# Performance work log

Hardware: AMD Instinct MI355X
Metric: run time of the kernel (lower is better)

Reference implementation:

```python
import jax, jax.numpy as jnp
import numpy as np

N = 20000        # nodes
E = 320000       # directed edges (before self-loops)
HEADS = 4
IN_DIM = 256
HID = [256, 128]
ZD = [128, 64]
S = 10           # num_samples in reparameterize
REAL_MIN = 2.2e-10
THETA_MAX = 1000.0
KMIN, KMAX = 0.1, 1000.0
SLOPE = 0.2      # GATConv leaky_relu negative_slope


def setup_inputs() -> dict:
    key = jax.random.key(0)
    ks = jax.random.split(key, 24)
    f32 = jnp.float32
    def p(k, shape, scale):
        return jax.random.normal(k, shape, dtype=f32) * scale
    inp = {}
    inp["x"] = jax.random.normal(ks[0], (N, IN_DIM), dtype=f32)
    inp["edge_index"] = jax.random.randint(ks[1], (2, E), 0, N)
    # layer 0: GAT 256 -> 4 heads x 64 (concat = 256)
    inp["gatW0"] = p(ks[2], (HID[0], IN_DIM), 0.06)
    inp["asrc0"] = p(ks[3], (HEADS, HID[0] // HEADS), 0.1)
    inp["adst0"] = p(ks[4], (HEADS, HID[0] // HEADS), 0.1)
    inp["gatb0"] = p(ks[5], (HID[0],), 0.02)
    inp["fcW0"] = p(ks[6], (ZD[0], HID[0]), 0.06)
    inp["fcb0"] = p(ks[7], (ZD[0],), 0.02)
    inp["shW0"] = p(ks[8], (ZD[0], ZD[0]), 0.08)
    inp["shb0"] = p(ks[9], (ZD[0],), 0.02)
    inp["scW0"] = p(ks[10], (ZD[0], ZD[0]), 0.08)
    inp["scb0"] = p(ks[11], (ZD[0],), 0.02)
    # layer 1: GAT 256 -> 4 heads x 32 (concat = 128)
    inp["gatW1"] = p(ks[12], (HID[1], HID[0]), 0.06)
    inp["asrc1"] = p(ks[13], (HEADS, HID[1] // HEADS), 0.1)
    inp["adst1"] = p(ks[14], (HEADS, HID[1] // HEADS), 0.1)
    inp["gatb1"] = p(ks[15], (HID[1],), 0.02)
    inp["fcW1"] = p(ks[16], (ZD[1], HID[1]), 0.06)
    inp["fcb1"] = p(ks[17], (ZD[1],), 0.02)
    inp["shW1"] = p(ks[18], (ZD[1], ZD[1]), 0.08)
    inp["shb1"] = p(ks[19], (ZD[1],), 0.02)
    inp["scW1"] = p(ks[20], (ZD[1], ZD[1]), 0.08)
    inp["scb1"] = p(ks[21], (ZD[1],), 0.02)
    # Weibull reparameterization noise eps ~ U(0,1), shape (S, z_dim, N)
    inp["eps0"] = jax.random.uniform(ks[22], (S, ZD[0], N), dtype=f32)
    inp["eps1"] = jax.random.uniform(ks[23], (S, ZD[1], N), dtype=f32)
    return inp


def _gat(x, src, dst, W, a_src, a_dst, b):
    """PyG GATConv (shared lin, concat heads, add_self_loops done by caller)."""
    n = x.shape[0]
    xw = (x @ W.T).reshape(n, HEADS, -1)            # [N, H, C]
    s = (xw * a_src[None]).sum(-1)                  # [N, H] alpha_src
    d = (xw * a_dst[None]).sum(-1)                  # [N, H] alpha_dst
    e = s[src] + d[dst]                             # [E, H]
    e = jnp.where(e > 0, e, SLOPE * e)              # leaky_relu
    m = jax.lax.stop_gradient(jax.ops.segment_max(e, dst, num_segments=n))
    ex = jnp.exp(e - m[dst])
    den = jax.ops.segment_sum(ex, dst, num_segments=n)
    alpha = ex / (den[dst] + 1e-16)                 # segment softmax over in-edges
    out = jax.ops.segment_sum(alpha[:, :, None] * xw[src], dst, num_segments=n)
    return out.reshape(n, -1) + b                   # [N, H*C]


def _reparam(k, l, eps):
    # theta = l * (-log(max(1-eps, real_min)))^(1/k), mean over samples, clamp
    lm = jnp.log(jnp.maximum(1.0 - eps, REAL_MIN))  # [S, z, N]
    theta = l[None] * jnp.power(-lm, 1.0 / k[None])
    return jnp.clip(theta.mean(0), REAL_MIN, THETA_MAX)


def _right(h, Wk, bk, Wl, bl, eps):
    k = jnp.clip(jax.nn.softplus(h @ Wk.T + bk).T, KMIN, KMAX)      # [z, N]
    l = jnp.maximum(jax.nn.softplus(h @ Wl.T + bl).T, REAL_MIN)     # [z, N]
    l = l / jnp.exp(jax.lax.lgamma(1.0 + 1.0 / k))
    return _reparam(k, l, eps), k, l


def reference(x, edge_index, gatW0, asrc0, adst0, gatb0, fcW0, fcb0, shW0, shb0,
              scW0, scb0, gatW1, asrc1, adst1, gatb1, fcW1, fcb1, shW1, shb1,
              scW1, scb1, eps0, eps1):
    n = x.shape[0]
    loops = jnp.arange(n)
    src = jnp.concatenate([edge_index[0], loops])   # GATConv add_self_loops
    dst = jnp.concatenate([edge_index[1], loops])
    h0 = _gat(x, src, dst, gatW0, asrc0, adst0, gatb0)
    z0 = jax.nn.softplus(h0 @ fcW0.T + fcb0)
    h1 = _gat(h0, src, dst, gatW1, asrc1, adst1, gatb1)
    z1 = jax.nn.softplus(h1 @ fcW1.T + fcb1)
    theta1, k1, l1 = _right(z1, shW1, shb1, scW1, scb1, eps1)
    theta0, k0, l0 = _right(z0, shW0, shb0, scW0, scb0, eps0)
    return (theta0, theta1, k0, k1, l0, l1)
```

## Files before the change

### kernel.cpp

```cpp
#include <hip/hip_runtime.h>
#include <math.h>

#define N_NODES 20000
#define E_EDGES 320000
#define NHEADS 4
#define RMIN 2.2e-10f
#define THETA_MAX 1000.0f
#define SLOPE 0.2f

__device__ __forceinline__ float softplus_f(float x) {
    return fmaxf(x, 0.0f) + log1pf(expf(-fabsf(x)));
}

__global__ __launch_bounds__(256) void count_kernel(const int* __restrict__ dst,
                                                    int* __restrict__ deg) {
    int e = blockIdx.x * 256 + threadIdx.x;
    if (e < E_EDGES) atomicAdd(&deg[dst[e]], 1);
}

__global__ __launch_bounds__(256) void scan_kernel(const int* __restrict__ deg,
                                                   int* __restrict__ rowptr,
                                                   int* __restrict__ cursor) {
    __shared__ int part[256];
    int t = threadIdx.x;
    const int CH = (N_NODES + 255) / 256;
    int base = t * CH;
    int sum = 0;
    for (int i = 0; i < CH; ++i) {
        int idx = base + i;
        if (idx < N_NODES) sum += deg[idx];
    }
    part[t] = sum;
    __syncthreads();
    for (int off = 1; off < 256; off <<= 1) {
        int v = (t >= off) ? part[t - off] : 0;
        __syncthreads();
        part[t] += v;
        __syncthreads();
    }
    int run = (t == 0) ? 0 : part[t - 1];
    for (int i = 0; i < CH; ++i) {
        int idx = base + i;
        if (idx < N_NODES) {
            rowptr[idx] = run;
            cursor[idx] = run;
            run += deg[idx];
        }
    }
    if (t == 255) rowptr[N_NODES] = run;
}

__global__ __launch_bounds__(256) void scatter_kernel(const int* __restrict__ src,
                                                      const int* __restrict__ dst,
                                                      int* __restrict__ cursor,
                                                      int* __restrict__ csr) {
    int e = blockIdx.x * 256 + threadIdx.x;
    if (e < E_EDGES) {
        int p = atomicAdd(&cursor[dst[e]], 1);
        csr[p] = src[e];
    }
}

template <int MODE, bool TRANS>
__global__ __launch_bounds__(256) void gemm_kernel(const float* __restrict__ A,
                                                   const float* __restrict__ W,
                                                   const float* __restrict__ bias,
                                                   float* __restrict__ out,
                                                   int M, int K, int NO) {
    __shared__ float As[16][68];
    __shared__ float Bs[16][68];
    int tid = threadIdx.x;
    int tx = tid & 15, ty = tid >> 4;
    int bm = blockIdx.x * 64;
    int bn = blockIdx.y * 64;
    float acc[4][4] = {};
    for (int k0 = 0; k0 < K; k0 += 16) {
        {
            int m = tid >> 2;
            int kk0 = (tid & 3) * 4;
            int row = bm + m;
            float4 v = make_float4(0.f, 0.f, 0.f, 0.f);
            if (row < M) v = *(const float4*)(A + (size_t)row * K + k0 + kk0);
            As[kk0 + 0][m] = v.x; As[kk0 + 1][m] = v.y;
            As[kk0 + 2][m] = v.z; As[kk0 + 3][m] = v.w;
        }
        {
            int o = tid >> 2;
            int kk0 = (tid & 3) * 4;
            float4 v = *(const float4*)(W + (size_t)(bn + o) * K + k0 + kk0);
            Bs[kk0 + 0][o] = v.x; Bs[kk0 + 1][o] = v.y;
            Bs[kk0 + 2][o] = v.z; Bs[kk0 + 3][o] = v.w;
        }
        __syncthreads();
#pragma unroll
        for (int kk = 0; kk < 16; ++kk) {
            float a[4], b[4];
            *(float4*)a = *(const float4*)(&As[kk][ty * 4]);
            *(float4*)b = *(const float4*)(&Bs[kk][tx * 4]);
#pragma unroll
            for (int i = 0; i < 4; ++i)
#pragma unroll
                for (int j = 0; j < 4; ++j) acc[i][j] += a[i] * b[j];
        }
        __syncthreads();
    }
    int r0 = bm + ty * 4;
    int c0 = bn + tx * 4;
    float bv[4] = {0.f, 0.f, 0.f, 0.f};
    if (MODE != 0) *(float4*)bv = *(const float4*)(bias + c0);
    float vals[4][4];
#pragma unroll
    for (int i = 0; i < 4; ++i)
#pragma unroll
        for (int j = 0; j < 4; ++j) {
            float v = acc[i][j];
            if (MODE == 1) v = softplus_f(v + bv[j]);
            else if (MODE == 2) { v = softplus_f(v + bv[j]); v = fminf(fmaxf(v, 0.1f), 1000.0f); }
            else if (MODE == 3) { v = fmaxf(softplus_f(v + bv[j]), RMIN); }
            vals[i][j] = v;
        }
    if (!TRANS) {
#pragma unroll
        for (int i = 0; i < 4; ++i) {
            int row = r0 + i;
            if (row < M) *(float4*)(out + (size_t)row * NO + c0) = *(float4*)vals[i];
        }
    } else {
        if (r0 + 3 < M) {
#pragma unroll
            for (int j = 0; j < 4; ++j) {
                float col[4] = {vals[0][j], vals[1][j], vals[2][j], vals[3][j]};
                *(float4*)(out + (size_t)(c0 + j) * M + r0) = *(float4*)col;
            }
        } else {
#pragma unroll
            for (int i = 0; i < 4; ++i) {
                int row = r0 + i;
                if (row < M)
#pragma unroll
                    for (int j = 0; j < 4; ++j) out[(size_t)(c0 + j) * M + row] = vals[i][j];
            }
        }
    }
}

template <int F, int CPER>
__global__ __launch_bounds__(256) void sd_kernel(const float* __restrict__ xw,
                                                 const float* __restrict__ asrc,
                                                 const float* __restrict__ adst,
                                                 float* __restrict__ s,
                                                 float* __restrict__ d) {
    int wave = threadIdx.x >> 6;
    int lane = threadIdx.x & 63;
    int n = blockIdx.x * 4 + wave;
    if (n >= N_NODES) return;
    float ss[NHEADS] = {0, 0, 0, 0}, dd[NHEADS] = {0, 0, 0, 0};
#pragma unroll
    for (int j = 0; j < F / 64; ++j) {
        int c = j * 64 + lane;
        int h = c / CPER;
        int cc = c % CPER;
        float v = xw[(size_t)n * F + c];
        ss[h] += v * asrc[h * CPER + cc];
        dd[h] += v * adst[h * CPER + cc];
    }
#pragma unroll
    for (int off = 32; off > 0; off >>= 1) {
#pragma unroll
        for (int h = 0; h < NHEADS; ++h) {
            ss[h] += __shfl_xor(ss[h], off, 64);
            dd[h] += __shfl_xor(dd[h], off, 64);
        }
    }
    if (lane == 0) {
#pragma unroll
        for (int h = 0; h < NHEADS; ++h) {
            s[n * NHEADS + h] = ss[h];
            d[n * NHEADS + h] = dd[h];
        }
    }
}

template <int F, int CPER>
__global__ __launch_bounds__(256) void agg_kernel(const float* __restrict__ xw,
                                                  const float* __restrict__ s,
                                                  const float* __restrict__ d,
                                                  const int* __restrict__ rowptr,
                                                  const int* __restrict__ csr,
                                                  const float* __restrict__ bias,
                                                  float* __restrict__ out) {
    int wave = threadIdx.x >> 6;
    int lane = threadIdx.x & 63;
    int n = blockIdx.x * 4 + wave;
    if (n >= N_NODES) return;
    constexpr int J = F / 64;
    float dh[NHEADS], shh[NHEADS];
#pragma unroll
    for (int h = 0; h < NHEADS; ++h) {
        dh[h] = d[n * NHEADS + h];
        shh[h] = s[n * NHEADS + h];
    }
    float den[NHEADS], w[NHEADS], acc[J];
#pragma unroll
    for (int h = 0; h < NHEADS; ++h) {
        float e = shh[h] + dh[h];
        e = e > 0.f ? e : SLOPE * e;
        w[h] = expf(e);
        den[h] = w[h];
    }
#pragma unroll
    for (int j = 0; j < J; ++j) {
        int c = j * 64 + lane;
        acc[j] = w[c / CPER] * xw[(size_t)n * F + c];
    }
    int beg = rowptr[n], end = rowptr[n + 1];
    for (int idx = beg; idx < end; ++idx) {
        int srcn = csr[idx];
#pragma unroll
        for (int h = 0; h < NHEADS; ++h) {
            float e = s[srcn * NHEADS + h] + dh[h];
            e = e > 0.f ? e : SLOPE * e;
            w[h] = expf(e);
            den[h] += w[h];
        }
#pragma unroll
        for (int j = 0; j < J; ++j) {
            int c = j * 64 + lane;
            acc[j] += w[c / CPER] * xw[(size_t)srcn * F + c];
        }
    }
#pragma unroll
    for (int j = 0; j < J; ++j) {
        int c = j * 64 + lane;
        out[(size_t)n * F + c] = acc[j] / (den[c / CPER] + 1e-16f) + bias[c];
    }
}

__global__ __launch_bounds__(256) void theta_kernel(const float* __restrict__ eps,
                                                    const float* __restrict__ kptr,
                                                    float* __restrict__ lptr,
                                                    float* __restrict__ theta, int ZN) {
    int i = blockIdx.x * 256 + threadIdx.x;
    if (i >= ZN) return;
    float k = kptr[i];
    float invk = 1.0f / k;
    float lg = expf(lgammaf(1.0f + invk));
    float l = lptr[i] / lg;
    lptr[i] = l;
    float acc = 0.0f;
#pragma unroll
    for (int ss = 0; ss < 10; ++ss) {
        float u = eps[(size_t)ss * ZN + i];
        float v = -logf(fmaxf(1.0f - u, RMIN));
        acc += exp2f(log2f(v) * invk);
    }
    float th = l * acc * 0.1f;
    th = fminf(fmaxf(th, RMIN), THETA_MAX);
    theta[i] = th;
}

extern "C" void kernel_launch(void* const* d_in, const int* in_sizes, int n_in,
                              void* d_out, int out_size, void* d_ws, size_t ws_size,
                              hipStream_t stream) {
    const float* x     = (const float*)d_in[0];
    const int*   eidx  = (const int*)d_in[1];
    const float* gatW0 = (const float*)d_in[2];
    const float* asrc0 = (const float*)d_in[3];
    const float* adst0 = (const float*)d_in[4];
    const float* gatb0 = (const float*)d_in[5];
    const float* fcW0  = (const float*)d_in[6];
    const float* fcb0  = (const float*)d_in[7];
    const float* shW0  = (const float*)d_in[8];
    const float* shb0  = (const float*)d_in[9];
    const float* scW0  = (const float*)d_in[10];
    const float* scb0  = (const float*)d_in[11];
    const float* gatW1 = (const float*)d_in[12];
    const float* asrc1 = (const float*)d_in[13];
    const float* adst1 = (const float*)d_in[14];
    const float* gatb1 = (const float*)d_in[15];
    const float* fcW1  = (const float*)d_in[16];
    const float* fcb1  = (const float*)d_in[17];
    const float* shW1  = (const float*)d_in[18];
    const float* shb1  = (const float*)d_in[19];
    const float* scW1  = (const float*)d_in[20];
    const float* scb1  = (const float*)d_in[21];
    const float* eps0  = (const float*)d_in[22];
    const float* eps1  = (const float*)d_in[23];

    const int* e_src = eidx;
    const int* e_dst = eidx + E_EDGES;

    size_t off = 0;
    auto carve = [&](size_t elems) {
        void* p = (char*)d_ws + off;
        off += ((elems * 4 + 255) / 256) * 256;
        return p;
    };
    float* xw0 = (float*)carve(20000u * 256);
    float* h0  = (float*)carve(20000u * 256);
    float* z0  = (float*)carve(20000u * 128);
    float* xw1 = (float*)carve(20000u * 128);
    float* h1  = (float*)carve(20000u * 128);
    float* z1  = (float*)carve(20000u * 64);
    float* s0  = (float*)carve(20000u * 4);
    float* d0  = (float*)carve(20000u * 4);
    float* s1  = (float*)carve(20000u * 4);
    float* d1  = (float*)carve(20000u * 4);
    int* deg    = (int*)carve(20000);
    int* rowptr = (int*)carve(20001);
    int* cursor = (int*)carve(20000);
    int* csr    = (int*)carve(E_EDGES);

    float* out    = (float*)d_out;
    float* theta0 = out;
    float* theta1 = out + 2560000;
    float* k0     = out + 3840000;
    float* k1     = out + 6400000;
    float* l0     = out + 7680000;
    float* l1     = out + 10240000;

    const int M = N_NODES;
    dim3 blk(256);

    (void)hipMemsetAsync(deg, 0, N_NODES * sizeof(int), stream);
    count_kernel<<<(E_EDGES + 255) / 256, blk, 0, stream>>>(e_dst, deg);
    scan_kernel<<<1, blk, 0, stream>>>(deg, rowptr, cursor);
    scatter_kernel<<<(E_EDGES + 255) / 256, blk, 0, stream>>>(e_src, e_dst, cursor, csr);

    gemm_kernel<0, false><<<dim3(313, 4), blk, 0, stream>>>(x, gatW0, nullptr, xw0, M, 256, 256);
    sd_kernel<256, 64><<<5000, blk, 0, stream>>>(xw0, asrc0, adst0, s0, d0);
    agg_kernel<256, 64><<<5000, blk, 0, stream>>>(xw0, s0, d0, rowptr, csr, gatb0, h0);
    gemm_kernel<1, false><<<dim3(313, 2), blk, 0, stream>>>(h0, fcW0, fcb0, z0, M, 256, 128);

    gemm_kernel<0, false><<<dim3(313, 2), blk, 0, stream>>>(h0, gatW1, nullptr, xw1, M, 256, 128);
    sd_kernel<128, 32><<<5000, blk, 0, stream>>>(xw1, asrc1, adst1, s1, d1);
    agg_kernel<128, 32><<<5000, blk, 0, stream>>>(xw1, s1, d1, rowptr, csr, gatb1, h1);
    gemm_kernel<1, false><<<dim3(313, 1), blk, 0, stream>>>(h1, fcW1, fcb1, z1, M, 128, 64);

    gemm_kernel<2, true><<<dim3(313, 2), blk, 0, stream>>>(z0, shW0, shb0, k0, M, 128, 128);
    gemm_kernel<3, true><<<dim3(313, 2), blk, 0, stream>>>(z0, scW0, scb0, l0, M, 128, 128);
    gemm_kernel<2, true><<<dim3(313, 1), blk, 0, stream>>>(z1, shW1, shb1, k1, M, 64, 64);
    gemm_kernel<3, true><<<dim3(313, 1), blk, 0, stream>>>(z1, scW1, scb1, l1, M, 64, 64);

    theta_kernel<<<(2560000 + 255) / 256, blk, 0, stream>>>(eps0, k0, l0, theta0, 2560000);
    theta_kernel<<<(1280000 + 255) / 256, blk, 0, stream>>>(eps1, k1, l1, theta1, 1280000);
}
```

Baseline: 693.0 us.

## Enlarge GEMM tiles, vectorize GAT score/aggregation and theta kernels with fast math

The GEMM kernel moves to 128-row tiles with 8xTN register blocking, so each thread does more FMAs per shared-memory load and fewer blocks are launched. The attention score kernel now has each lane load a float4 or float2 and reduce within 16-lane head groups. The aggregation kernel gives each lane one head and a vector of features, and unrolls two edges per iteration to put more gathers in flight. The theta kernel handles four elements per thread with vector loads and uses __expf/__logf intrinsics, trading some accuracy for cheaper transcendentals.

Measured after the change: 729.9 us. 1.05x slower.

```diff
diff --git a/kernel.cpp b/kernel.cpp
--- a/kernel.cpp
+++ b/kernel.cpp
@@ -61,58 +61,84 @@
     }
 }
 
-template <int MODE, bool TRANS>
-__global__ __launch_bounds__(256) void gemm_kernel(const float* __restrict__ A,
-                                                   const float* __restrict__ W,
-                                                   const float* __restrict__ bias,
-                                                   float* __restrict__ out,
-                                                   int M, int K, int NO) {
-    __shared__ float As[16][68];
-    __shared__ float Bs[16][68];
+template <int MODE, bool TRANS, int BN>
+__global__ __launch_bounds__(256) void gemm_big(const float* __restrict__ A,
+                                                const float* __restrict__ W,
+                                                const float* __restrict__ bias,
+                                                float* __restrict__ out,
+                                                int M, int K, int NO) {
+    constexpr int TN = BN / 16;
+    __shared__ float As[16][132];
+    __shared__ float Bs[16][BN + 4];
     int tid = threadIdx.x;
     int tx = tid & 15, ty = tid >> 4;
-    int bm = blockIdx.x * 64;
-    int bn = blockIdx.y * 64;
-    float acc[4][4] = {};
+    int bm = blockIdx.x * 128;
+    int bn = blockIdx.y * BN;
+    float acc[8][TN] = {};
+
+    int am = tid >> 1;
+    int ak = (tid & 1) * 8;
+    int arow = bm + am;
+    bool aval = arow < M;
+    const float* Arow = A + (size_t)arow * K + ak;
+
+    int bo, bk;
+    if (BN == 128) { bo = tid >> 1; bk = (tid & 1) * 8; }
+    else           { bo = tid >> 2; bk = (tid & 3) * 4; }
+    const float* Wrow = W + (size_t)(bn + bo) * K + bk;
+
     for (int k0 = 0; k0 < K; k0 += 16) {
-        {
-            int m = tid >> 2;
-            int kk0 = (tid & 3) * 4;
-            int row = bm + m;
-            float4 v = make_float4(0.f, 0.f, 0.f, 0.f);
-            if (row < M) v = *(const float4*)(A + (size_t)row * K + k0 + kk0);
-            As[kk0 + 0][m] = v.x; As[kk0 + 1][m] = v.y;
-            As[kk0 + 2][m] = v.z; As[kk0 + 3][m] = v.w;
-        }
-        {
-            int o = tid >> 2;
-            int kk0 = (tid & 3) * 4;
-            float4 v = *(const float4*)(W + (size_t)(bn + o) * K + k0 + kk0);
-            Bs[kk0 + 0][o] = v.x; Bs[kk0 + 1][o] = v.y;
-            Bs[kk0 + 2][o] = v.z; Bs[kk0 + 3][o] = v.w;
+        float4 a0 = make_float4(0.f, 0.f, 0.f, 0.f), a1 = a0;
+        if (aval) {
+            a0 = *(const float4*)(Arow + k0);
+            a1 = *(const float4*)(Arow + k0 + 4);
+        }
+        As[ak + 0][am] = a0.x; As[ak + 1][am] = a0.y;
+        As[ak + 2][am] = a0.z; As[ak + 3][am] = a0.w;
+        As[ak + 4][am] = a1.x; As[ak + 5][am] = a1.y;
+        As[ak + 6][am] = a1.z; As[ak + 7][am] = a1.w;
+        if (BN == 128) {
+            float4 b0 = *(const float4*)(Wrow + k0);
+            float4 b1 = *(const float4*)(Wrow + k0 + 4);
+            Bs[bk + 0][bo] = b0.x; Bs[bk + 1][bo] = b0.y;
+            Bs[bk + 2][bo] = b0.z; Bs[bk + 3][bo] = b0.w;
+            Bs[bk + 4][bo] = b1.x; Bs[bk + 5][bo] = b1.y;
+            Bs[bk + 6][bo] = b1.z; Bs[bk + 7][bo] = b1.w;
+        } else {
+            float4 b0 = *(const float4*)(Wrow + k0);
+            Bs[bk + 0][bo] = b0.x; Bs[bk + 1][bo] = b0.y;
+            Bs[bk + 2][bo] = b0.z; Bs[bk + 3][bo] = b0.w;
         }
         __syncthreads();
 #pragma unroll
         for (int kk = 0; kk < 16; ++kk) {
-            float a[4], b[4];
-            *(float4*)a = *(const float4*)(&As[kk][ty * 4]);
-            *(float4*)b = *(const float4*)(&Bs[kk][tx * 4]);
-#pragma unroll
-            for (int i = 0; i < 4; ++i)
-#pragma unroll
-                for (int j = 0; j < 4; ++j) acc[i][j] += a[i] * b[j];
+            float a[8], b[TN];
+            *(float4*)(a) = *(const float4*)(&As[kk][ty * 8]);
+            *(float4*)(a + 4) = *(const float4*)(&As[kk][ty * 8 + 4]);
+            *(float4*)(b) = *(const float4*)(&Bs[kk][tx * TN]);
+            if (TN == 8) *(float4*)(b + 4) = *(const float4*)(&Bs[kk][tx * TN + 4]);
+#pragma unroll
+            for (int i = 0; i < 8; ++i)
+#pragma unroll
+                for (int j = 0; j < TN; ++j) acc[i][j] += a[i] * b[j];
         }
         __syncthreads();
     }
-    int r0 = bm + ty * 4;
-    int c0 = bn + tx * 4;
-    float bv[4] = {0.f, 0.f, 0.f, 0.f};
-    if (MODE != 0) *(float4*)bv = *(const float4*)(bias + c0);
-    float vals[4][4];
-#pragma unroll
-    for (int i = 0; i < 4; ++i)
-#pragma unroll
-        for (int j = 0; j < 4; ++j) {
+
+    int r0 = bm + ty * 8;
+    int c0 = bn + tx * TN;
+    float bv[TN];
+#pragma unroll
+    for (int j = 0; j < TN; ++j) bv[j] = 0.f;
+    if (MODE != 0) {
+        *(float4*)(bv) = *(const float4*)(bias + c0);
+        if (TN == 8) *(float4*)(bv + 4) = *(const float4*)(bias + c0 + 4);
+    }
+    float vals[8][TN];
+#pragma unroll
+    for (int i = 0; i < 8; ++i)
+#pragma unroll
+        for (int j = 0; j < TN; ++j) {
             float v = acc[i][j];
             if (MODE == 1) v = softplus_f(v + bv[j]);
             else if (MODE == 2) { v = softplus_f(v + bv[j]); v = fminf(fmaxf(v, 0.1f), 1000.0f); }
@@ -121,30 +147,35 @@
         }
     if (!TRANS) {
 #pragma unroll
-        for (int i = 0; i < 4; ++i) {
+        for (int i = 0; i < 8; ++i) {
             int row = r0 + i;
-            if (row < M) *(float4*)(out + (size_t)row * NO + c0) = *(float4*)vals[i];
+            if (row < M) {
+                *(float4*)(out + (size_t)row * NO + c0) = *(float4*)(vals[i]);
+                if (TN == 8) *(float4*)(out + (size_t)row * NO + c0 + 4) = *(float4*)(vals[i] + 4);
+            }
         }
     } else {
-        if (r0 + 3 < M) {
-#pragma unroll
-            for (int j = 0; j < 4; ++j) {
-                float col[4] = {vals[0][j], vals[1][j], vals[2][j], vals[3][j]};
-                *(float4*)(out + (size_t)(c0 + j) * M + r0) = *(float4*)col;
+        if (r0 + 7 < M) {
+#pragma unroll
+            for (int j = 0; j < TN; ++j) {
+                float c0v[4] = {vals[0][j], vals[1][j], vals[2][j], vals[3][j]};
+                float c1v[4] = {vals[4][j], vals[5][j], vals[6][j], vals[7][j]};
+                *(float4*)(out + (size_t)(c0 + j) * M + r0) = *(float4*)c0v;
+                *(float4*)(out + (size_t)(c0 + j) * M + r0 + 4) = *(float4*)c1v;
             }
         } else {
 #pragma unroll
-            for (int i = 0; i < 4; ++i) {
+            for (int i = 0; i < 8; ++i) {
                 int row = r0 + i;
                 if (row < M)
 #pragma unroll
-                    for (int j = 0; j < 4; ++j) out[(size_t)(c0 + j) * M + row] = vals[i][j];
+                    for (int j = 0; j < TN; ++j) out[(size_t)(c0 + j) * M + row] = vals[i][j];
             }
         }
     }
 }
 
-template <int F, int CPER>
+template <int F>
 __global__ __launch_bounds__(256) void sd_kernel(const float* __restrict__ xw,
                                                  const float* __restrict__ asrc,
                                                  const float* __restrict__ adst,
@@ -154,34 +185,33 @@
     int lane = threadIdx.x & 63;
     int n = blockIdx.x * 4 + wave;
     if (n >= N_NODES) return;
-    float ss[NHEADS] = {0, 0, 0, 0}, dd[NHEADS] = {0, 0, 0, 0};
-#pragma unroll
-    for (int j = 0; j < F / 64; ++j) {
-        int c = j * 64 + lane;
-        int h = c / CPER;
-        int cc = c % CPER;
-        float v = xw[(size_t)n * F + c];
-        ss[h] += v * asrc[h * CPER + cc];
-        dd[h] += v * adst[h * CPER + cc];
-    }
-#pragma unroll
-    for (int off = 32; off > 0; off >>= 1) {
-#pragma unroll
-        for (int h = 0; h < NHEADS; ++h) {
-            ss[h] += __shfl_xor(ss[h], off, 64);
-            dd[h] += __shfl_xor(dd[h], off, 64);
-        }
-    }
-    if (lane == 0) {
-#pragma unroll
-        for (int h = 0; h < NHEADS; ++h) {
-            s[n * NHEADS + h] = ss[h];
-            d[n * NHEADS + h] = dd[h];
-        }
-    }
-}
-
-template <int F, int CPER>
+    float ss, dd;
+    if (F == 256) {
+        float4 v = *(const float4*)(xw + (size_t)n * 256 + lane * 4);
+        float4 as = *(const float4*)(asrc + lane * 4);
+        float4 ad = *(const float4*)(adst + lane * 4);
+        ss = v.x * as.x + v.y * as.y + v.z * as.z + v.w * as.w;
+        dd = v.x * ad.x + v.y * ad.y + v.z * ad.z + v.w * ad.w;
+    } else {
+        float2 v = *(const float2*)(xw + (size_t)n * 128 + lane * 2);
+        float2 as = *(const float2*)(asrc + lane * 2);
+        float2 ad = *(const float2*)(adst + lane * 2);
+        ss = v.x * as.x + v.y * as.y;
+        dd = v.x * ad.x + v.y * ad.y;
+    }
+#pragma unroll
+    for (int off = 8; off > 0; off >>= 1) {
+        ss += __shfl_xor(ss, off, 64);
+        dd += __shfl_xor(dd, off, 64);
+    }
+    if ((lane & 15) == 0) {
+        int h = lane >> 4;
+        s[n * NHEADS + h] = ss;
+        d[n * NHEADS + h] = dd;
+    }
+}
+
+template <int F>
 __global__ __launch_bounds__(256) void agg_kernel(const float* __restrict__ xw,
                                                   const float* __restrict__ s,
                                                   const float* __restrict__ d,
@@ -193,46 +223,79 @@
     int lane = threadIdx.x & 63;
     int n = blockIdx.x * 4 + wave;
     if (n >= N_NODES) return;
-    constexpr int J = F / 64;
-    float dh[NHEADS], shh[NHEADS];
-#pragma unroll
-    for (int h = 0; h < NHEADS; ++h) {
-        dh[h] = d[n * NHEADS + h];
-        shh[h] = s[n * NHEADS + h];
-    }
-    float den[NHEADS], w[NHEADS], acc[J];
-#pragma unroll
-    for (int h = 0; h < NHEADS; ++h) {
-        float e = shh[h] + dh[h];
-        e = e > 0.f ? e : SLOPE * e;
-        w[h] = expf(e);
-        den[h] = w[h];
-    }
-#pragma unroll
-    for (int j = 0; j < J; ++j) {
-        int c = j * 64 + lane;
-        acc[j] = w[c / CPER] * xw[(size_t)n * F + c];
-    }
+    int h = lane >> 4;
+    float dh = d[n * 4 + h];
+    float eself = s[n * 4 + h] + dh;
+    eself = eself > 0.f ? eself : SLOPE * eself;
+    float wself = __expf(eself);
+    float den = wself;
+
     int beg = rowptr[n], end = rowptr[n + 1];
-    for (int idx = beg; idx < end; ++idx) {
-        int srcn = csr[idx];
-#pragma unroll
-        for (int h = 0; h < NHEADS; ++h) {
-            float e = s[srcn * NHEADS + h] + dh[h];
-            e = e > 0.f ? e : SLOPE * e;
-            w[h] = expf(e);
-            den[h] += w[h];
-        }
-#pragma unroll
-        for (int j = 0; j < J; ++j) {
-            int c = j * 64 + lane;
-            acc[j] += w[c / CPER] * xw[(size_t)srcn * F + c];
-        }
-    }
-#pragma unroll
-    for (int j = 0; j < J; ++j) {
-        int c = j * 64 + lane;
-        out[(size_t)n * F + c] = acc[j] / (den[c / CPER] + 1e-16f) + bias[c];
+    if (F == 256) {
+        const float4* xw4 = (const float4*)xw;
+        float4 v = xw4[(size_t)n * 64 + lane];
+        float4 acc = make_float4(wself * v.x, wself * v.y, wself * v.z, wself * v.w);
+        int idx = beg;
+        for (; idx + 1 < end; idx += 2) {
+            int s0 = csr[idx], s1 = csr[idx + 1];
+            float e0 = s[s0 * 4 + h] + dh;
+            float e1 = s[s1 * 4 + h] + dh;
+            e0 = e0 > 0.f ? e0 : SLOPE * e0;
+            e1 = e1 > 0.f ? e1 : SLOPE * e1;
+            float w0 = __expf(e0);
+            float w1 = __expf(e1);
+            float4 v0 = xw4[(size_t)s0 * 64 + lane];
+            float4 v1 = xw4[(size_t)s1 * 64 + lane];
+            den += w0 + w1;
+            acc.x += w0 * v0.x; acc.y += w0 * v0.y; acc.z += w0 * v0.z; acc.w += w0 * v0.w;
+            acc.x += w1 * v1.x; acc.y += w1 * v1.y; acc.z += w1 * v1.z; acc.w += w1 * v1.w;
+        }
+        if (idx < end) {
+            int s0 = csr[idx];
+            float e0 = s[s0 * 4 + h] + dh;
+            e0 = e0 > 0.f ? e0 : SLOPE * e0;
+            float w0 = __expf(e0);
+            float4 v0 = xw4[(size_t)s0 * 64 + lane];
+            den += w0;
+            acc.x += w0 * v0.x; acc.y += w0 * v0.y; acc.z += w0 * v0.z; acc.w += w0 * v0.w;
+        }
+        float inv = 1.0f / (den + 1e-16f);
+        float4 bv = *(const float4*)(bias + lane * 4);
+        float4 o = make_float4(acc.x * inv + bv.x, acc.y * inv + bv.y,
+                               acc.z * inv + bv.z, acc.w * inv + bv.w);
+        *(float4*)(out + (size_t)n * 256 + lane * 4) = o;
+    } else {
+        const float2* xw2 = (const float2*)xw;
+        float2 v = xw2[(size_t)n * 64 + lane];
+        float2 acc = make_float2(wself * v.x, wself * v.y);
+        int idx = beg;
+        for (; idx + 1 < end; idx += 2) {
+            int s0 = csr[idx], s1 = csr[idx + 1];
+            float e0 = s[s0 * 4 + h] + dh;
+            float e1 = s[s1 * 4 + h] + dh;
+            e0 = e0 > 0.f ? e0 : SLOPE * e0;
+            e1 = e1 > 0.f ? e1 : SLOPE * e1;
+            float w0 = __expf(e0);
+            float w1 = __expf(e1);
+            float2 v0 = xw2[(size_t)s0 * 64 + lane];
+            float2 v1 = xw2[(size_t)s1 * 64 + lane];
+            den += w0 + w1;
+            acc.x += w0 * v0.x; acc.y += w0 * v0.y;
+            acc.x += w1 * v1.x; acc.y += w1 * v1.y;
+        }
+        if (idx < end) {
+            int s0 = csr[idx];
+            float e0 = s[s0 * 4 + h] + dh;
+            e0 = e0 > 0.f ? e0 : SLOPE * e0;
+            float w0 = __expf(e0);
+            float2 v0 = xw2[(size_t)s0 * 64 + lane];
+            den += w0;
+            acc.x += w0 * v0.x; acc.y += w0 * v0.y;
+        }
+        float inv = 1.0f / (den + 1e-16f);
+        float2 bv = *(const float2*)(bias + lane * 2);
+        float2 o = make_float2(acc.x * inv + bv.x, acc.y * inv + bv.y);
+        *(float2*)(out + (size_t)n * 128 + lane * 2) = o;
     }
 }
 
@@ -240,23 +303,39 @@
                                                     const float* __restrict__ kptr,
                                                     float* __restrict__ lptr,
                                                     float* __restrict__ theta, int ZN) {
-    int i = blockIdx.x * 256 + threadIdx.x;
-    if (i >= ZN) return;
-    float k = kptr[i];
-    float invk = 1.0f / k;
-    float lg = expf(lgammaf(1.0f + invk));
-    float l = lptr[i] / lg;
-    lptr[i] = l;
-    float acc = 0.0f;
+    int idx = blockIdx.x * 256 + threadIdx.x;
+    int base = idx * 4;
+    if (base >= ZN) return;
+    float4 k4 = *(const float4*)(kptr + base);
+    float4 l4 = *(const float4*)(lptr + base);
+    float kk[4] = {k4.x, k4.y, k4.z, k4.w};
+    float ll[4] = {l4.x, l4.y, l4.z, l4.w};
+    float invk[4], acc[4];
+#pragma unroll
+    for (int c = 0; c < 4; ++c) {
+        invk[c] = 1.0f / kk[c];
+        ll[c] = ll[c] / __expf(lgammaf(1.0f + invk[c]));
+        acc[c] = 0.0f;
+    }
 #pragma unroll
     for (int ss = 0; ss < 10; ++ss) {
-        float u = eps[(size_t)ss * ZN + i];
-        float v = -logf(fmaxf(1.0f - u, RMIN));
-        acc += exp2f(log2f(v) * invk);
-    }
-    float th = l * acc * 0.1f;
-    th = fminf(fmaxf(th, RMIN), THETA_MAX);
-    theta[i] = th;
+        float4 u4 = *(const float4*)(eps + (size_t)ss * ZN + base);
+        float uu[4] = {u4.x, u4.y, u4.z, u4.w};
+#pragma unroll
+        for (int c = 0; c < 4; ++c) {
+            float w = fmaxf(1.0f - uu[c], RMIN);
+            float v = -__logf(w);
+            acc[c] += __expf(invk[c] * __logf(v));
+        }
+    }
+    float th[4];
+#pragma unroll
+    for (int c = 0; c < 4; ++c) {
+        float t = ll[c] * acc[c] * 0.1f;
+        th[c] = fminf(fmaxf(t, RMIN), THETA_MAX);
+    }
+    *(float4*)(theta + base) = make_float4(th[0], th[1], th[2], th[3]);
+    *(float4*)(lptr + base) = make_float4(ll[0], ll[1], ll[2], ll[3]);
 }
 
 extern "C" void kernel_launch(void* const* d_in, const int* in_sizes, int n_in,
@@ -327,21 +406,21 @@
     scan_kernel<<<1, blk, 0, stream>>>(deg, rowptr, cursor);
     scatter_kernel<<<(E_EDGES + 255) / 256, blk, 0, stream>>>(e_src, e_dst, cursor, csr);
 
-    gemm_kernel<0, false><<<dim3(313, 4), blk, 0, stream>>>(x, gatW0, nullptr, xw0, M, 256, 256);
-    sd_kernel<256, 64><<<5000, blk, 0, stream>>>(xw0, asrc0, adst0, s0, d0);
-    agg_kernel<256, 64><<<5000, blk, 0, stream>>>(xw0, s0, d0, rowptr, csr, gatb0, h0);
-    gemm_kernel<1, false><<<dim3(313, 2), blk, 0, stream>>>(h0, fcW0, fcb0, z0, M, 256, 128);
-
-    gemm_kernel<0, false><<<dim3(313, 2), blk, 0, stream>>>(h0, gatW1, nullptr, xw1, M, 256, 128);
-    sd_kernel<128, 32><<<5000, blk, 0, stream>>>(xw1, asrc1, adst1, s1, d1);
-    agg_kernel<128, 32><<<5000, blk, 0, stream>>>(xw1, s1, d1, rowptr, csr, gatb1, h1);
-    gemm_kernel<1, false><<<dim3(313, 1), blk, 0, stream>>>(h1, fcW1, fcb1, z1, M, 128, 64);
-
-    gemm_kernel<2, true><<<dim3(313, 2), blk, 0, stream>>>(z0, shW0, shb0, k0, M, 128, 128);
-    gemm_kernel<3, true><<<dim3(313, 2), blk, 0, stream>>>(z0, scW0, scb0, l0, M, 128, 128);
-    gemm_kernel<2, true><<<dim3(313, 1), blk, 0, stream>>>(z1, shW1, shb1, k1, M, 64, 64);
-    gemm_kernel<3, true><<<dim3(313, 1), blk, 0, stream>>>(z1, scW1, scb1, l1, M, 64, 64);
-
-    theta_kernel<<<(2560000 + 255) / 256, blk, 0, stream>>>(eps0, k0, l0, theta0, 2560000);
-    theta_kernel<<<(1280000 + 255) / 256, blk, 0, stream>>>(eps1, k1, l1, theta1, 1280000);
-}
+    gemm_big<0, false, 128><<<dim3(157, 2), blk, 0, stream>>>(x, gatW0, nullptr, xw0, M, 256, 256);
+    sd_kernel<256><<<5000, blk, 0, stream>>>(xw0, asrc0, adst0, s0, d0);
+    agg_kernel<256><<<5000, blk, 0, stream>>>(xw0, s0, d0, rowptr, csr, gatb0, h0);
+    gemm_big<1, false, 128><<<dim3(157, 1), blk, 0, stream>>>(h0, fcW0, fcb0, z0, M, 256, 128);
+
+    gemm_big<0, false, 128><<<dim3(157, 1), blk, 0, stream>>>(h0, gatW1, nullptr, xw1, M, 256, 128);
+    sd_kernel<128><<<5000, blk, 0, stream>>>(xw1, asrc1, adst1, s1, d1);
+    agg_kernel<128><<<5000, blk, 0, stream>>>(xw1, s1, d1, rowptr, csr, gatb1, h1);
+    gemm_big<1, false, 64><<<dim3(157, 1), blk, 0, stream>>>(h1, fcW1, fcb1, z1, M, 128, 64);
+
+    gemm_big<2, true, 128><<<dim3(157, 1), blk, 0, stream>>>(z0, shW0, shb0, k0, M, 128, 128);
+    gemm_big<3, true, 128><<<dim3(157, 1), blk, 0, stream>>>(z0, scW0, scb0, l0, M, 128, 128);
+    gemm_big<2, true, 64><<<dim3(157, 1), blk, 0, stream>>>(z1, shW1, shb1, k1, M, 64, 64);
+    gemm_big<3, true, 64><<<dim3(157, 1), blk, 0, stream>>>(z1, scW1, scb1, l1, M, 64, 64);
+
+    theta_kernel<<<(640000 + 255) / 256, blk, 0, stream>>>(eps0, k0, l0, theta0, 2560000);
+    theta_kernel<<<(320000 + 255) / 256, blk, 0, stream>>>(eps1, k1, l1, theta1, 1280000);
+}
```
